# Performance work log

Measured on AMD Instinct MI355X. Metric: run time of the kernel, lower is better.

The kernel has to match this reference:

```python
import jax, jax.numpy as jnp
import numpy as np
from jax import lax

# Dims: mel, reduction factor, encoder dim, prenet hidden, attention dim,
# attention-RNN units, decoder-RNN units, location-conv filters/kernel.
MEL, R, ENC, PRE, ATTN, ARNN, DRNN, FILT, K = 80, 2, 512, 256, 128, 1024, 1024, 32, 31
B, T_ENC, T_DEC = 64, 200, 400


def setup_inputs() -> dict:
    key = jax.random.key(0)
    ks = jax.random.split(key, 16)
    g = lambda i, shape: jax.random.normal(ks[i], shape, jnp.float32) * 0.02
    return {
        "encoder_outputs": jax.random.normal(ks[0], (B, T_ENC, ENC), jnp.float32),
        "inputs": jax.random.normal(ks[1], (B, T_DEC, MEL), jnp.float32),
        # prenet
        "W_pre1": g(2, (PRE, MEL)), "b_pre1": jnp.zeros((PRE,), jnp.float32),
        "W_pre2": g(3, (PRE, PRE)), "b_pre2": jnp.zeros((PRE,), jnp.float32),
        # memory layer (no bias)
        "W_mem": g(4, (ATTN, ENC)),
        # attention LSTMCell: input = prenet(256) + context(512)
        "Wih_a": g(5, (4 * ARNN, PRE + ENC)), "Whh_a": g(6, (4 * ARNN, ARNN)),
        "bih_a": jnp.zeros((4 * ARNN,), jnp.float32), "bhh_a": jnp.zeros((4 * ARNN,), jnp.float32),
        # location-sensitive attention
        "W_q": g(7, (ATTN, ARNN)),
        "W_conv": g(8, (FILT, 1, K)),
        "W_loc": g(9, (ATTN, FILT)),
        "v": g(10, (ATTN,)),
        # decoder LSTMCell: input = attn_rnn_h(1024) + context(512)
        "Wih_d": g(11, (4 * DRNN, ARNN + ENC)), "Whh_d": g(12, (4 * DRNN, DRNN)),
        "bih_d": jnp.zeros((4 * DRNN,), jnp.float32), "bhh_d": jnp.zeros((4 * DRNN,), jnp.float32),
        # output projections from cat(decoder_h, context) = 1536
        "W_mel": g(13, (MEL * R, DRNN + ENC)), "b_mel": jnp.zeros((MEL * R,), jnp.float32),
        "W_stop": g(14, (1, DRNN + ENC)), "b_stop": jnp.zeros((1,), jnp.float32),
    }


def _lstm(x, h, c, Wih, Whh, bih, bhh):
    # torch LSTMCell gate order: i, f, g, o
    gates = x @ Wih.T + bih + h @ Whh.T + bhh
    i, f, gg, o = jnp.split(gates, 4, axis=-1)
    c2 = jax.nn.sigmoid(f) * c + jax.nn.sigmoid(i) * jnp.tanh(gg)
    return jax.nn.sigmoid(o) * jnp.tanh(c2), c2


def _forward(encoder_outputs, inputs, W_pre1, b_pre1, W_pre2, b_pre2, W_mem,
             Wih_a, Whh_a, bih_a, bhh_a, W_q, W_conv, W_loc, v,
             Wih_d, Whh_d, bih_d, bhh_d, W_mel, b_mel, W_stop, b_stop):
    b, t_enc, _ = encoder_outputs.shape
    steps = inputs.shape[1] // R
    pm = encoder_outputs @ W_mem.T  # (B, T_enc, ATTN) processed memory
    # teacher-forced inputs: step 0 uses zeros, step k uses inputs[:, k*R-1]
    tf = inputs[:, R - 1::R, :][:, :steps - 1, :]
    dec_in = jnp.concatenate([jnp.zeros((b, 1, MEL), inputs.dtype), tf], axis=1).transpose(1, 0, 2)
    pad = (K - 1) // 2

    def step(carry, x):
        ah, ac, dh, dc, ctx, aw = carry
        # prenet (dropout disabled / eval mode)
        p = jax.nn.relu(jax.nn.relu(x @ W_pre1.T + b_pre1) @ W_pre2.T + b_pre2)
        ah, ac = _lstm(jnp.concatenate([p, ctx], -1), ah, ac, Wih_a, Whh_a, bih_a, bhh_a)
        # location feature from previous alignment: conv1d over time
        loc = lax.conv_general_dilated(aw[:, None, :], W_conv, (1,), [(pad, pad)],
                                       dimension_numbers=("NCH", "OIH", "NCH"))  # (B, FILT, T_enc)
        feat = jnp.tanh((ah @ W_q.T)[:, None, :] + jnp.einsum("bft,af->bta", loc, W_loc) + pm)
        align = jax.nn.softmax(jnp.einsum("bta,a->bt", feat, v), axis=-1)  # (B, T_enc)
        ctx = jnp.einsum("bt,btd->bd", align, encoder_outputs)  # (B, ENC)
        dh, dc = _lstm(jnp.concatenate([ah, ctx], -1), dh, dc, Wih_d, Whh_d, bih_d, bhh_d)
        proj = jnp.concatenate([dh, ctx], -1)  # (B, DRNN+ENC)
        mel = (proj @ W_mel.T + b_mel).reshape(b, R, MEL)
        stop = jax.nn.sigmoid(proj @ W_stop.T + b_stop)[:, 0]
        return (ah, ac, dh, dc, ctx, align), (mel, stop, align)

    z = lambda d: jnp.zeros((b, d), encoder_outputs.dtype)
    carry0 = (z(ARNN), z(ARNN), z(DRNN), z(DRNN), z(ENC),
              jnp.zeros((b, t_enc), encoder_outputs.dtype))
    _, (mels, stops, aligns) = lax.scan(step, carry0, dec_in)
    mel_outputs = mels.transpose(1, 0, 2, 3).reshape(b, steps * R, MEL)  # (B, T_dec, MEL)
    stop_tokens = jnp.repeat(stops.transpose(1, 0), R, axis=1)  # (B, T_dec)
    attn_scores = aligns.transpose(1, 0, 2)  # (B, steps, T_enc)
    return mel_outputs, stop_tokens, attn_scores


def reference(encoder_outputs, inputs, W_pre1, b_pre1, W_pre2, b_pre2, W_mem,
              Wih_a, Whh_a, bih_a, bhh_a, W_q, W_conv, W_loc, v,
              Wih_d, Whh_d, bih_d, bhh_d, W_mel, b_mel, W_stop, b_stop):
    return _forward(encoder_outputs, inputs, W_pre1, b_pre1, W_pre2, b_pre2, W_mem,
                    Wih_a, Whh_a, bih_a, bhh_a, W_q, W_conv, W_loc, v,
                    Wih_d, Whh_d, bih_d, bhh_d, W_mel, b_mel, W_stop, b_stop)
```

## Files before the change

### kernel.cpp

```cpp
#include <hip/hip_runtime.h>
#include <hip/hip_bf16.h>
#include <stdint.h>

#define STEPS  200
#define KA     1792
#define KD     2560
#define SLOT   (64*2560)

using bf16 = __bf16;
typedef __bf16 bf16x8 __attribute__((ext_vector_type(8)));
typedef float  f32x4  __attribute__((ext_vector_type(4)));
typedef unsigned int       u32;
typedef unsigned long long u64;

union U2h { u32 u; bf16 h[2]; };

#define MFMA16(a,b,c) __builtin_amdgcn_mfma_f32_16x16x32_bf16((a),(b),(c),0,0,0)

__device__ __forceinline__ float sigf(float x){ return 1.f/(1.f+__expf(-x)); }
__device__ __forceinline__ float tanhf_(float x){
  float ax = fabsf(x);
  float e  = __expf(-2.f*ax);
  float t  = (1.f-e)/(1.f+e);
  return x < 0.f ? -t : t;
}

__global__ void cvt_kernel(const float* __restrict__ s, bf16* __restrict__ d, int n){
  int i = blockIdx.x*256 + threadIdx.x;
  if (i < n) d[i] = (bf16)s[i];
}
__global__ void cvt_pad_kernel(const float* __restrict__ s, bf16* __restrict__ d,
                               int rows, int cin, int cout){
  int i = blockIdx.x*256 + threadIdx.x;
  if (i >= rows*cout) return;
  int r = i / cout, c = i % cout;
  d[i] = (bf16)(c < cin ? s[(size_t)r*cin + c] : 0.f);
}
__global__ void build_wa_pack(const float* __restrict__ Wiha, const float* __restrict__ Whha,
                              bf16* __restrict__ d){
  int i = blockIdx.x*256 + threadIdx.x;
  if (i >= 4096*1792) return;
  int r = i / 1792, k = i % 1792;
  int q = r >> 5, g = (r >> 3) & 3, j = r & 7;
  int orig = g*1024 + q*8 + j;
  float v = (k < 768) ? Wiha[(size_t)orig*768 + k] : Whha[(size_t)orig*1024 + (k - 768)];
  d[i] = (bf16)v;
}
__global__ void build_wd_pack(const float* __restrict__ Wihd, const float* __restrict__ Whhd,
                              bf16* __restrict__ d){
  int i = blockIdx.x*256 + threadIdx.x;
  if (i >= 4096*2560) return;
  int r = i / 2560, k = i % 2560;
  int q = r >> 5, g = (r >> 3) & 3, j = r & 7;
  int orig = g*1024 + q*8 + j;
  float v;
  if (k < 512)        v = Wihd[(size_t)orig*1536 + 1024 + k];
  else if (k < 1536)  v = Wihd[(size_t)orig*1536 + (k - 512)];
  else                v = Whhd[(size_t)orig*1024 + (k - 1536)];
  d[i] = (bf16)v;
}
__global__ void build_wmelcat(const float* __restrict__ Wmel, const float* __restrict__ Wstop,
                              bf16* __restrict__ d){
  int i = blockIdx.x*256 + threadIdx.x;
  if (i >= 176*1536) return;
  int r = i / 1536, c = i % 1536;
  float v = (r < 160) ? Wmel[(size_t)r*1536 + c] : (r == 160 ? Wstop[c] : 0.f);
  d[i] = (bf16)v;
}
__global__ void build_misc2(const float* biha, const float* bhha, float* biasa2,
                            const float* bihd, const float* bhhd, float* biasd2,
                            const float* bmel, const float* bstop, float* bias176,
                            const float* Wloc, float* wlocT){
  int i = blockIdx.x*256 + threadIdx.x;
  if (i < 4096){
    int q = i >> 5, g = (i >> 3) & 3, j = i & 7;
    int orig = g*1024 + q*8 + j;
    biasa2[i] = biha[orig] + bhha[orig];
  } else if (i < 8192){
    int r = i - 4096;
    int q = r >> 5, g = (r >> 3) & 3, j = r & 7;
    int orig = g*1024 + q*8 + j;
    biasd2[r] = bihd[orig] + bhhd[orig];
  } else if (i < 8192+176){
    int j = i - 8192;
    bias176[j] = (j < 160) ? bmel[j] : (j == 160 ? bstop[0] : 0.f);
  } else if (i < 8192+176+4096){
    int t = i - 8368;
    int f = t >> 7, a = t & 127;
    wlocT[t] = Wloc[a*32 + f];
  }
}
__global__ void build_decin(const float* __restrict__ inp, bf16* __restrict__ d){
  int i = blockIdx.x*256 + threadIdx.x;
  if (i >= 12800*96) return;
  int row = i / 96, c = i % 96;
  int s = row >> 6, b = row & 63;
  float v = 0.f;
  if (c < 80 && s > 0) v = inp[((size_t)b*400 + (2*s - 1))*80 + c];
  d[i] = (bf16)v;
}

template<int ACT, int OBF>
__global__ __launch_bounds__(256)
void gemm_k(const bf16* __restrict__ A, const bf16* __restrict__ Bm,
            const float* __restrict__ bias, float* __restrict__ Cf,
            bf16* __restrict__ Cb, int M, int N, int K, int MT)
{
  int wid = blockIdx.x*4 + (threadIdx.x >> 6);
  if (wid >= MT*(N >> 4)) return;
  int wm = wid % MT, wn = wid / MT;
  int l = threadIdx.x & 63, lo = l & 15, hi = l >> 4;
  const bf16* Bp = Bm + (size_t)(wn*16 + lo)*K + hi*8;
  const bf16* Ap = A  + (size_t)(wm*64 + lo)*K + hi*8;
  f32x4 acc0 = {0,0,0,0}, acc1 = {0,0,0,0}, acc2 = {0,0,0,0}, acc3 = {0,0,0,0};
  for (int k = 0; k < K; k += 32){
    bf16x8 bb = *(const bf16x8*)(Bp + k);
    bf16x8 a0 = *(const bf16x8*)(Ap + k);
    bf16x8 a1 = *(const bf16x8*)(Ap + (size_t)16*K + k);
    bf16x8 a2 = *(const bf16x8*)(Ap + (size_t)32*K + k);
    bf16x8 a3 = *(const bf16x8*)(Ap + (size_t)48*K + k);
    acc0 = MFMA16(a0, bb, acc0);
    acc1 = MFMA16(a1, bb, acc1);
    acc2 = MFMA16(a2, bb, acc2);
    acc3 = MFMA16(a3, bb, acc3);
  }
  int n = wn*16 + lo;
  float bv = bias ? bias[n] : 0.f;
  int m0 = wm*64 + hi*4;
  #pragma unroll
  for (int mt = 0; mt < 4; ++mt){
    f32x4 av = (mt==0)?acc0:(mt==1)?acc1:(mt==2)?acc2:acc3;
    #pragma unroll
    for (int r = 0; r < 4; ++r){
      float v = av[r] + bv;
      if (ACT) v = fmaxf(v, 0.f);
      size_t idx = (size_t)(m0 + mt*16 + r)*N + n;
      if (OBF) Cb[idx] = (bf16)v; else Cf[idx] = v;
    }
  }
}

__global__ __launch_bounds__(1024)
void gates_step(const bf16* __restrict__ pall,
                const bf16* __restrict__ Wa, const bf16* __restrict__ Wd2,
                const float* __restrict__ biasa2, const float* __restrict__ biasd2,
                const bf16* __restrict__ slotPrev, bf16* __restrict__ slotCur,
                float* __restrict__ aC, float* __restrict__ dC,
                bf16* __restrict__ proj, int i, int doA, int doD)
{
  const bool isA = blockIdx.x < 128;
  if (isA ? !doA : !doD) return;
  const int tid = threadIdx.x;
  const int l = tid & 63, lo = l & 15, hi = l >> 4;
  const int wv = tid >> 6;
  const int kq = wv & 3;
  const int m0 = (wv >> 2) * 16;
  const int bq = isA ? blockIdx.x : blockIdx.x - 128;
  const int n0 = bq * 32;
  const int K  = isA ? KA : KD;
  const int JQ = isA ? 14 : 20;
  const bf16* Wg = isA ? Wa : Wd2;
  const float* bias2 = isA ? biasa2 : biasd2;
  float* Cst = (isA ? aC : dC) + (size_t)bq*64*8;

  __shared__ float red[4][64][33];

  const bf16* Wp0  = Wg + (size_t)(n0 +      lo)*K + hi*8;
  const bf16* Wp1  = Wg + (size_t)(n0 + 16 + lo)*K + hi*8;
  const bf16* Xrow = slotPrev + (size_t)(m0 + lo)*2560 + hi*8;
  const bf16* Prow = pall + ((size_t)i*64 + m0 + lo)*256 + hi*8;
  const int kbase = kq * (K >> 2);
  f32x4 acc0 = {0,0,0,0}, acc1 = {0,0,0,0};
  #pragma unroll 4
  for (int jj = 0; jj < JQ; ++jj){
    int k = kbase + jj*32;
    const bf16* ap;
    if (isA) ap = (k < 256) ? (Prow + k) : (Xrow + (k - 256));
    else     ap = Xrow + k;
    bf16x8 a  = *(const bf16x8*)ap;
    bf16x8 b0 = *(const bf16x8*)(Wp0 + k);
    bf16x8 b1 = *(const bf16x8*)(Wp1 + k);
    acc0 = MFMA16(a, b0, acc0);
    acc1 = MFMA16(a, b1, acc1);
  }
  #pragma unroll
  for (int r = 0; r < 4; ++r){
    red[kq][m0 + hi*4 + r][lo]      = acc0[r];
    red[kq][m0 + hi*4 + r][16 + lo] = acc1[r];
  }
  __syncthreads();
  if (tid < 256){
    const int b  = tid >> 2;
    const int jp = (tid & 3)*2;
    U2h hp;
    #pragma unroll
    for (int t = 0; t < 2; ++t){
      int j = jp + t;
      float gi = red[0][b][     j] + red[1][b][     j] + red[2][b][     j] + red[3][b][     j] + bias2[n0 +      j];
      float gf = red[0][b][ 8 + j] + red[1][b][ 8 + j] + red[2][b][ 8 + j] + red[3][b][ 8 + j] + bias2[n0 +  8 + j];
      float gg = red[0][b][16 + j] + red[1][b][16 + j] + red[2][b][16 + j] + red[3][b][16 + j] + bias2[n0 + 16 + j];
      float go = red[0][b][24 + j] + red[1][b][24 + j] + red[2][b][24 + j] + red[3][b][24 + j] + bias2[n0 + 24 + j];
      float* cp = Cst + b*8 + j;
      float c = sigf(gf)*(*cp) + sigf(gi)*tanhf_(gg);
      float h = sigf(go)*tanhf_(c);
      *cp = c;
      hp.h[t] = (bf16)h;
    }
    const int u = bq*8 + jp;
    if (isA){
      *(u32*)(slotCur + (size_t)b*2560 + 512 + u) = hp.u;
    } else {
      *(u32*)(slotCur + (size_t)b*2560 + 1536 + u) = hp.u;
      *(u32*)(proj + ((size_t)(i-1)*64 + b)*1536 + u) = hp.u;
    }
  }
}

__global__ __launch_bounds__(1024)
void attn_step(const bf16* __restrict__ Wqb, const float* __restrict__ Wconv,
               const float* __restrict__ wlocTg, const float* __restrict__ vvp,
               const float* __restrict__ pm, const bf16* __restrict__ enc_bf,
               const float* __restrict__ alignPrev,
               bf16* __restrict__ slotCur, bf16* __restrict__ proj,
               float* __restrict__ out_attn, int i)
{
  const int tid = threadIdx.x;
  const int l = tid & 63, wv = tid >> 6;
  const int b = blockIdx.x;

  __shared__ __align__(16) bf16 ahs[1024];
  __shared__ float locb[200][32];
  __shared__ float awl[256];
  __shared__ float qp[1024];
  __shared__ float qv[128];
  __shared__ float es[200];
  __shared__ float sred[16];
  __shared__ float wlocT[32][128];
  __shared__ float credx[4][256];
  __shared__ float credy[4][256];

  if (tid < 256) awl[tid] = 0.f;
  if (i > 0 && tid < 200) awl[tid] = alignPrev[((size_t)b*200 + (i-1))*200 + tid];
  for (int it = tid; it < 4096; it += 1024)
    wlocT[it >> 7][it & 127] = wlocTg[it];
  if (tid < 128)
    *(bf16x8*)(&ahs[tid*8]) = *(const bf16x8*)(slotCur + (size_t)b*2560 + 512 + tid*8);
  __syncthreads();
  for (int it = tid; it < 6400; it += 1024){
    int f = it & 31, tl = it >> 5;
    float s = 0.f;
    #pragma unroll
    for (int j = 0; j < 31; ++j){
      int tt = tl + j - 15;
      if ((unsigned)tt < 200u) s += awl[tt]*Wconv[f*31+j];
    }
    locb[tl][f] = s;
  }
  {
    int a = tid & 127, seg = tid >> 7;
    const bf16* wr = Wqb + (size_t)a*1024 + seg*128;
    float s = 0.f;
    #pragma unroll
    for (int k2 = 0; k2 < 128; k2 += 8){
      bf16x8 x = *(const bf16x8*)(&ahs[seg*128 + k2]);
      bf16x8 y = *(const bf16x8*)(wr + k2);
      #pragma unroll
      for (int e = 0; e < 8; ++e) s += (float)x[e]*(float)y[e];
    }
    qp[tid] = s;
  }
  __syncthreads();
  if (tid < 128){
    float s = 0.f;
    #pragma unroll
    for (int sg = 0; sg < 8; ++sg) s += qp[tid + sg*128];
    qv[tid] = s;
  }
  __syncthreads();
  for (int tl = wv; tl < 200; tl += 16){
    const float* pmrow = pm + ((size_t)b*200 + tl)*128;
    const float* lrow  = locb[tl];
    float s = 0.f;
    #pragma unroll
    for (int half = 0; half < 2; ++half){
      int a = l + half*64;
      float x = qv[a] + pmrow[a];
      #pragma unroll
      for (int f = 0; f < 32; ++f) x += lrow[f]*wlocT[f][a];
      s += vvp[a]*tanhf_(x);
    }
    #pragma unroll
    for (int o = 32; o; o >>= 1) s += __shfl_xor(s, o);
    if (l == 0) es[tl] = s;
  }
  __syncthreads();
  {
    float e0 = (tid < 200) ? es[tid] : -3.0e38f;
    float m = e0;
    #pragma unroll
    for (int o = 32; o; o >>= 1) m = fmaxf(m, __shfl_xor(m, o));
    if (l == 0) sred[wv] = m;
    __syncthreads();
    m = fmaxf(fmaxf(sred[0],sred[1]), fmaxf(sred[2],sred[3]));
    float p = (tid < 200) ? __expf(e0 - m) : 0.f;
    float ss = p;
    #pragma unroll
    for (int o = 32; o; o >>= 1) ss += __shfl_xor(ss, o);
    __syncthreads();
    if (l == 0) sred[wv] = ss;
    __syncthreads();
    ss = sred[0]+sred[1]+sred[2]+sred[3];
    float aval = p / ss;
    if (tid < 200){
      awl[tid] = aval;
      out_attn[((size_t)b*200 + i)*200 + tid] = aval;
    }
  }
  __syncthreads();
  {
    const int col = tid & 255, tq = tid >> 8;
    const u32* ep = (const u32*)(enc_bf + (size_t)b*102400) + col;
    float x0 = 0.f, y0 = 0.f;
    const int t0 = tq*50;
    #pragma unroll 5
    for (int t = t0; t < t0 + 50; ++t){
      U2h w; w.u = ep[(size_t)t*256];
      float al = awl[t];
      x0 += al*(float)w.h[0];
      y0 += al*(float)w.h[1];
    }
    credx[tq][col] = x0;
    credy[tq][col] = y0;
  }
  __syncthreads();
  if (tid < 256){
    float sx = credx[0][tid]+credx[1][tid]+credx[2][tid]+credx[3][tid];
    float sy = credy[0][tid]+credy[1][tid]+credy[2][tid]+credy[3][tid];
    U2h cb; cb.h[0] = (bf16)sx; cb.h[1] = (bf16)sy;
    *((u32*)(slotCur + (size_t)b*2560) + tid) = cb.u;
    *((u32*)(proj + ((size_t)i*64 + b)*1536 + 1024) + tid) = cb.u;
  }
}

__global__ void scatter_out(const float* __restrict__ mt_, float* __restrict__ out){
  int i = blockIdx.x*256 + threadIdx.x;
  const int NMEL = 12800*160;
  if (i < NMEL){
    int sb = i / 160, j = i % 160;
    int s = sb >> 6, b = sb & 63;
    int r = j / 80, mm = j % 80;
    out[((size_t)b*400 + 2*s + r)*80 + mm] = mt_[(size_t)sb*176 + j];
  } else if (i < NMEL + 12800){
    int sb = i - NMEL;
    int s = sb >> 6, b = sb & 63;
    float st = sigf(mt_[(size_t)sb*176 + 160]);
    float* so = out + 2048000;
    so[(size_t)b*400 + 2*s]     = st;
    so[(size_t)b*400 + 2*s + 1] = st;
  }
}

extern "C" void kernel_launch(void* const* d_in, const int* in_sizes, int n_in,
                              void* d_out, int out_size, void* d_ws, size_t ws_size,
                              hipStream_t stream)
{
  const float* enc   = (const float*)d_in[0];
  const float* inp   = (const float*)d_in[1];
  const float* Wpre1 = (const float*)d_in[2];
  const float* bpre1 = (const float*)d_in[3];
  const float* Wpre2 = (const float*)d_in[4];
  const float* bpre2 = (const float*)d_in[5];
  const float* Wmem  = (const float*)d_in[6];
  const float* Wiha  = (const float*)d_in[7];
  const float* Whha  = (const float*)d_in[8];
  const float* biha  = (const float*)d_in[9];
  const float* bhha  = (const float*)d_in[10];
  const float* Wq    = (const float*)d_in[11];
  const float* Wconv = (const float*)d_in[12];
  const float* Wloc  = (const float*)d_in[13];
  const float* vv    = (const float*)d_in[14];
  const float* Wihd  = (const float*)d_in[15];
  const float* Whhd  = (const float*)d_in[16];
  const float* bihd  = (const float*)d_in[17];
  const float* bhhd  = (const float*)d_in[18];
  const float* Wmel  = (const float*)d_in[19];
  const float* bmel  = (const float*)d_in[20];
  const float* Wstop = (const float*)d_in[21];
  const float* bstop = (const float*)d_in[22];
  float* out = (float*)d_out;

  char* pp = (char*)d_ws;
  auto carve = [&](size_t bytes)->char*{
    char* r = (char*)(((uintptr_t)pp + 255) & ~(uintptr_t)255);
    pp = r + bytes;
    return r;
  };
  bf16*  enc_bf  = (bf16*) carve((size_t)64*200*512*2);
  float* pm      = (float*)carve((size_t)64*200*128*4);
  bf16*  decin   = (bf16*) carve((size_t)12800*96*2);
  bf16*  h1      = (bf16*) carve((size_t)12800*256*2);
  bf16*  pall    = (bf16*) carve((size_t)12800*256*2);
  bf16*  Wp1b    = (bf16*) carve((size_t)256*96*2);
  bf16*  Wp2b    = (bf16*) carve((size_t)256*256*2);
  bf16*  Wmemb   = (bf16*) carve((size_t)128*512*2);
  bf16*  Wqb     = (bf16*) carve((size_t)128*1024*2);
  bf16*  Wca     = (bf16*) carve((size_t)4096*KA*2);
  bf16*  Wcd2    = (bf16*) carve((size_t)4096*KD*2);
  bf16*  Wmc     = (bf16*) carve((size_t)176*1536*2);
  float* biasa2  = (float*)carve(4096*4);
  float* biasd2  = (float*)carve(4096*4);
  float* bias176 = (float*)carve(176*4);
  float* wlocTg  = (float*)carve(4096*4);
  bf16*  proj    = (bf16*) carve((size_t)12800*1536*2);
  float* meltmp  = (float*)carve((size_t)12800*176*4);
  float* aC  = (float*)carve((size_t)128*64*8*4);
  float* dC  = (float*)carve((size_t)128*64*8*4);
  size_t zbytes = (size_t)((char*)dC + (size_t)128*64*8*4 - (char*)aC);
  bf16*  ring = (bf16*)carve((size_t)202*SLOT*2);
  hipMemsetAsync(aC, 0, zbytes, stream);
  hipMemsetAsync(ring, 0, (size_t)2*SLOT*2, stream);

  cvt_kernel<<<(6553600+255)/256,256,0,stream>>>(enc,   enc_bf, 6553600);
  cvt_kernel<<<(131072+255)/256, 256,0,stream>>>(Wq,    Wqb,    131072);
  cvt_kernel<<<(65536+255)/256,  256,0,stream>>>(Wmem,  Wmemb,  65536);
  cvt_kernel<<<(65536+255)/256,  256,0,stream>>>(Wpre2, Wp2b,   65536);
  cvt_pad_kernel<<<(256*96+255)/256,256,0,stream>>>(Wpre1, Wp1b, 256, 80, 96);
  build_wa_pack<<<(4096*1792+255)/256,256,0,stream>>>(Wiha, Whha, Wca);
  build_wd_pack<<<(4096*2560+255)/256,256,0,stream>>>(Wihd, Whhd, Wcd2);
  build_wmelcat<<<(176*1536+255)/256,256,0,stream>>>(Wmel, Wstop, Wmc);
  build_misc2<<<(8368+4096+255)/256,256,0,stream>>>(biha,bhha,biasa2, bihd,bhhd,biasd2,
                                                    bmel,bstop,bias176, Wloc, wlocTg);
  build_decin<<<(12800*96+255)/256,256,0,stream>>>(inp, decin);

  gemm_k<1,1><<<800,256,0,stream>>>(decin, Wp1b, bpre1, nullptr, h1, 12800,256,96, 200);
  gemm_k<1,1><<<800,256,0,stream>>>(h1, Wp2b, bpre2, nullptr, pall, 12800,256,256, 200);
  gemm_k<0,0><<<400,256,0,stream>>>(enc_bf, Wmemb, nullptr, pm, nullptr, 12800,128,512, 200);

  float* out_attn = out + 2073600;
  for (int i = 0; i <= STEPS; ++i){
    const bf16* slotPrev = ring + (size_t)i*SLOT;
    bf16*       slotCur  = ring + (size_t)(i+1)*SLOT;
    gates_step<<<256,1024,0,stream>>>(pall, Wca, Wcd2, biasa2, biasd2,
                                      slotPrev, slotCur, aC, dC, proj,
                                      i, i < STEPS ? 1 : 0, i > 0 ? 1 : 0);
    if (i < STEPS)
      attn_step<<<64,1024,0,stream>>>(Wqb, Wconv, wlocTg, vv, pm, enc_bf,
                                      out_attn, slotCur, proj, out_attn, i);
  }

  gemm_k<0,0><<<550,256,0,stream>>>(proj, Wmc, bias176, meltmp, nullptr, 12800,176,1536, 200);
  scatter_out<<<(12800*160+12800+255)/256,256,0,stream>>>(meltmp, out);
}
```

Measured before the change: 19.76 ms.

## Halve gate-tile width to double gates_step blocks; split attn context accumulators

```diff
diff --git a/kernel.cpp b/kernel.cpp
--- a/kernel.cpp
+++ b/kernel.cpp
@@ -41,8 +41,8 @@
   int i = blockIdx.x*256 + threadIdx.x;
   if (i >= 4096*1792) return;
   int r = i / 1792, k = i % 1792;
-  int q = r >> 5, g = (r >> 3) & 3, j = r & 7;
-  int orig = g*1024 + q*8 + j;
+  int q2 = r >> 4, g = (r >> 2) & 3, j = r & 3;
+  int orig = g*1024 + q2*4 + j;
   float v = (k < 768) ? Wiha[(size_t)orig*768 + k] : Whha[(size_t)orig*1024 + (k - 768)];
   d[i] = (bf16)v;
 }
@@ -51,8 +51,8 @@
   int i = blockIdx.x*256 + threadIdx.x;
   if (i >= 4096*2560) return;
   int r = i / 2560, k = i % 2560;
-  int q = r >> 5, g = (r >> 3) & 3, j = r & 7;
-  int orig = g*1024 + q*8 + j;
+  int q2 = r >> 4, g = (r >> 2) & 3, j = r & 3;
+  int orig = g*1024 + q2*4 + j;
   float v;
   if (k < 512)        v = Wihd[(size_t)orig*1536 + 1024 + k];
   else if (k < 1536)  v = Wihd[(size_t)orig*1536 + (k - 512)];
@@ -73,13 +73,13 @@
                             const float* Wloc, float* wlocT){
   int i = blockIdx.x*256 + threadIdx.x;
   if (i < 4096){
-    int q = i >> 5, g = (i >> 3) & 3, j = i & 7;
-    int orig = g*1024 + q*8 + j;
+    int q2 = i >> 4, g = (i >> 2) & 3, j = i & 3;
+    int orig = g*1024 + q2*4 + j;
     biasa2[i] = biha[orig] + bhha[orig];
   } else if (i < 8192){
     int r = i - 4096;
-    int q = r >> 5, g = (r >> 3) & 3, j = r & 7;
-    int orig = g*1024 + q*8 + j;
+    int q2 = r >> 4, g = (r >> 2) & 3, j = r & 3;
+    int orig = g*1024 + q2*4 + j;
     biasd2[r] = bihd[orig] + bhhd[orig];
   } else if (i < 8192+176){
     int j = i - 8192;
@@ -140,7 +140,7 @@
   }
 }
 
-__global__ __launch_bounds__(1024)
+__global__ __launch_bounds__(1024, 8)
 void gates_step(const bf16* __restrict__ pall,
                 const bf16* __restrict__ Wa, const bf16* __restrict__ Wd2,
                 const float* __restrict__ biasa2, const float* __restrict__ biasd2,
@@ -148,29 +148,28 @@
                 float* __restrict__ aC, float* __restrict__ dC,
                 bf16* __restrict__ proj, int i, int doA, int doD)
 {
-  const bool isA = blockIdx.x < 128;
+  const bool isA = blockIdx.x < 256;
   if (isA ? !doA : !doD) return;
   const int tid = threadIdx.x;
   const int l = tid & 63, lo = l & 15, hi = l >> 4;
   const int wv = tid >> 6;
   const int kq = wv & 3;
   const int m0 = (wv >> 2) * 16;
-  const int bq = isA ? blockIdx.x : blockIdx.x - 128;
-  const int n0 = bq * 32;
+  const int bq = isA ? blockIdx.x : blockIdx.x - 256;
+  const int n0 = bq * 16;
   const int K  = isA ? KA : KD;
   const int JQ = isA ? 14 : 20;
   const bf16* Wg = isA ? Wa : Wd2;
   const float* bias2 = isA ? biasa2 : biasd2;
-  float* Cst = (isA ? aC : dC) + (size_t)bq*64*8;
-
-  __shared__ float red[4][64][33];
-
-  const bf16* Wp0  = Wg + (size_t)(n0 +      lo)*K + hi*8;
-  const bf16* Wp1  = Wg + (size_t)(n0 + 16 + lo)*K + hi*8;
+  float* Cst = (isA ? aC : dC) + (size_t)bq*64*4;
+
+  __shared__ float red[4][64][17];
+
+  const bf16* Wp0  = Wg + (size_t)(n0 + lo)*K + hi*8;
   const bf16* Xrow = slotPrev + (size_t)(m0 + lo)*2560 + hi*8;
   const bf16* Prow = pall + ((size_t)i*64 + m0 + lo)*256 + hi*8;
   const int kbase = kq * (K >> 2);
-  f32x4 acc0 = {0,0,0,0}, acc1 = {0,0,0,0};
+  f32x4 acc0 = {0,0,0,0};
   #pragma unroll 4
   for (int jj = 0; jj < JQ; ++jj){
     int k = kbase + jj*32;
@@ -179,39 +178,30 @@
     else     ap = Xrow + k;
     bf16x8 a  = *(const bf16x8*)ap;
     bf16x8 b0 = *(const bf16x8*)(Wp0 + k);
-    bf16x8 b1 = *(const bf16x8*)(Wp1 + k);
     acc0 = MFMA16(a, b0, acc0);
-    acc1 = MFMA16(a, b1, acc1);
   }
   #pragma unroll
-  for (int r = 0; r < 4; ++r){
-    red[kq][m0 + hi*4 + r][lo]      = acc0[r];
-    red[kq][m0 + hi*4 + r][16 + lo] = acc1[r];
-  }
+  for (int r = 0; r < 4; ++r)
+    red[kq][m0 + hi*4 + r][lo] = acc0[r];
   __syncthreads();
   if (tid < 256){
     const int b  = tid >> 2;
-    const int jp = (tid & 3)*2;
-    U2h hp;
-    #pragma unroll
-    for (int t = 0; t < 2; ++t){
-      int j = jp + t;
-      float gi = red[0][b][     j] + red[1][b][     j] + red[2][b][     j] + red[3][b][     j] + bias2[n0 +      j];
-      float gf = red[0][b][ 8 + j] + red[1][b][ 8 + j] + red[2][b][ 8 + j] + red[3][b][ 8 + j] + bias2[n0 +  8 + j];
-      float gg = red[0][b][16 + j] + red[1][b][16 + j] + red[2][b][16 + j] + red[3][b][16 + j] + bias2[n0 + 16 + j];
-      float go = red[0][b][24 + j] + red[1][b][24 + j] + red[2][b][24 + j] + red[3][b][24 + j] + bias2[n0 + 24 + j];
-      float* cp = Cst + b*8 + j;
-      float c = sigf(gf)*(*cp) + sigf(gi)*tanhf_(gg);
-      float h = sigf(go)*tanhf_(c);
-      *cp = c;
-      hp.h[t] = (bf16)h;
-    }
-    const int u = bq*8 + jp;
+    const int j4 = tid & 3;
+    float gi = red[0][b][     j4] + red[1][b][     j4] + red[2][b][     j4] + red[3][b][     j4] + bias2[n0 +      j4];
+    float gf = red[0][b][ 4 + j4] + red[1][b][ 4 + j4] + red[2][b][ 4 + j4] + red[3][b][ 4 + j4] + bias2[n0 +  4 + j4];
+    float gg = red[0][b][ 8 + j4] + red[1][b][ 8 + j4] + red[2][b][ 8 + j4] + red[3][b][ 8 + j4] + bias2[n0 +  8 + j4];
+    float go = red[0][b][12 + j4] + red[1][b][12 + j4] + red[2][b][12 + j4] + red[3][b][12 + j4] + bias2[n0 + 12 + j4];
+    float* cp = Cst + b*4 + j4;
+    float c = sigf(gf)*(*cp) + sigf(gi)*tanhf_(gg);
+    float h = sigf(go)*tanhf_(c);
+    *cp = c;
+    bf16 hb = (bf16)h;
+    const int u = bq*4 + j4;
     if (isA){
-      *(u32*)(slotCur + (size_t)b*2560 + 512 + u) = hp.u;
+      slotCur[(size_t)b*2560 + 512 + u] = hb;
     } else {
-      *(u32*)(slotCur + (size_t)b*2560 + 1536 + u) = hp.u;
-      *(u32*)(proj + ((size_t)(i-1)*64 + b)*1536 + u) = hp.u;
+      slotCur[(size_t)b*2560 + 1536 + u] = hb;
+      proj[((size_t)(i-1)*64 + b)*1536 + u] = hb;
     }
   }
 }
@@ -320,17 +310,18 @@
   {
     const int col = tid & 255, tq = tid >> 8;
     const u32* ep = (const u32*)(enc_bf + (size_t)b*102400) + col;
-    float x0 = 0.f, y0 = 0.f;
+    float x0 = 0.f, y0 = 0.f, x1 = 0.f, y1 = 0.f;
     const int t0 = tq*50;
     #pragma unroll 5
-    for (int t = t0; t < t0 + 50; ++t){
-      U2h w; w.u = ep[(size_t)t*256];
-      float al = awl[t];
-      x0 += al*(float)w.h[0];
-      y0 += al*(float)w.h[1];
-    }
-    credx[tq][col] = x0;
-    credy[tq][col] = y0;
+    for (int t = t0; t < t0 + 50; t += 2){
+      U2h w0; w0.u = ep[(size_t)t*256];
+      U2h w1; w1.u = ep[(size_t)(t+1)*256];
+      float a0 = awl[t], a1 = awl[t+1];
+      x0 += a0*(float)w0.h[0]; y0 += a0*(float)w0.h[1];
+      x1 += a1*(float)w1.h[0]; y1 += a1*(float)w1.h[1];
+    }
+    credx[tq][col] = x0 + x1;
+    credy[tq][col] = y0 + y1;
   }
   __syncthreads();
   if (tid < 256){
@@ -413,9 +404,9 @@
   float* wlocTg  = (float*)carve(4096*4);
   bf16*  proj    = (bf16*) carve((size_t)12800*1536*2);
   float* meltmp  = (float*)carve((size_t)12800*176*4);
-  float* aC  = (float*)carve((size_t)128*64*8*4);
-  float* dC  = (float*)carve((size_t)128*64*8*4);
-  size_t zbytes = (size_t)((char*)dC + (size_t)128*64*8*4 - (char*)aC);
+  float* aC  = (float*)carve((size_t)256*64*4*4);
+  float* dC  = (float*)carve((size_t)256*64*4*4);
+  size_t zbytes = (size_t)((char*)dC + (size_t)256*64*4*4 - (char*)aC);
   bf16*  ring = (bf16*)carve((size_t)202*SLOT*2);
   hipMemsetAsync(aC, 0, zbytes, stream);
   hipMemsetAsync(ring, 0, (size_t)2*SLOT*2, stream);
@@ -440,7 +431,7 @@
   for (int i = 0; i <= STEPS; ++i){
     const bf16* slotPrev = ring + (size_t)i*SLOT;
     bf16*       slotCur  = ring + (size_t)(i+1)*SLOT;
-    gates_step<<<256,1024,0,stream>>>(pall, Wca, Wcd2, biasa2, biasd2,
+    gates_step<<<512,1024,0,stream>>>(pall, Wca, Wcd2, biasa2, biasd2,
                                       slotPrev, slotCur, aC, dC, proj,
                                       i, i < STEPS ? 1 : 0, i > 0 ? 1 : 0);
     if (i < STEPS)
```

Result: no change. 20.11 ms (+1.8%).
